# Optimization experiments

Hardware: AMD Instinct MI355X
Metric: run time of the kernel (lower is better)

The kernel has to match this reference:

```python
import jax, jax.numpy as jnp
import numpy as np

B, S, D, H = 64, 256, 2048, 8
DH = D // H  # 256; NOTE: S must equal DH for the original module's broadcast to be valid
EPS = 1e-06


def setup_inputs() -> dict:
    key = jax.random.key(0)
    ks = jax.random.split(key, 8)
    s = 1.0 / np.sqrt(D)
    x = jax.random.normal(ks[0], (B, S, D), jnp.float32)
    Wq = jax.random.normal(ks[1], (D, D), jnp.float32) * s
    Wk = jax.random.normal(ks[2], (D, D), jnp.float32) * s
    Wv = jax.random.normal(ks[3], (D, D), jnp.float32) * s
    Wo = jax.random.normal(ks[4], (2 * D, D), jnp.float32) * (1.0 / np.sqrt(2 * D))
    bq = jnp.zeros((D,), jnp.float32)
    bk = jnp.zeros((D,), jnp.float32)
    bv = jnp.zeros((D,), jnp.float32)
    bo = jnp.zeros((D,), jnp.float32)
    gamma = jnp.ones((D,), jnp.float32)
    beta = jnp.zeros((D,), jnp.float32)
    return {"x": x, "Wq": Wq, "bq": bq, "Wk": Wk, "bk": bk, "Wv": Wv, "bv": bv,
            "Wo": Wo, "bo": bo, "gamma": gamma, "beta": beta}


def reference(x, Wq, bq, Wk, bk, Wv, bv, Wo, bo, gamma, beta):
    def split_heads(t):  # [B,S,D] -> [B,H,S,DH]
        return t.reshape(B, S, H, DH).transpose(0, 2, 1, 3)

    q_proj = x @ Wq + bq  # reused later as the residual projection
    q = jax.nn.elu(split_heads(q_proj)) + 1.0
    k = jax.nn.elu(split_heads(x @ Wk + bk)) + 1.0
    v = split_heads(x @ Wv + bv)

    key_sum = k.sum(axis=2, keepdims=True)  # [B,H,1,DH]
    # Original TF code broadcasts [B,H,S,S] / [B,H,1,DH]; valid because S == DH
    scores = jnp.einsum('bhqd,bhkd->bhqk', q, k) / (key_sum + EPS)
    attn = jnp.einsum('bhqk,bhkd->bhqd', scores, v)
    attn = attn.transpose(0, 2, 1, 3).reshape(B, S, D)

    summary = jnp.broadcast_to(attn.mean(axis=1, keepdims=True), (B, S, D))
    combined = jnp.concatenate([attn, summary], axis=-1) @ Wo + bo  # [B,S,D]
    # dropout is identity (training=False)

    z = q_proj + combined
    mu = z.mean(axis=-1, keepdims=True)
    var = z.var(axis=-1, keepdims=True)
    return (z - mu) / jnp.sqrt(var + EPS) * gamma + beta
```

## Files before the change

kernel.cpp:

```cpp
#include <hip/hip_runtime.h>
#include <hip/hip_bf16.h>

typedef __attribute__((ext_vector_type(8))) __bf16 bf16x8v;
typedef __attribute__((ext_vector_type(4))) float f32x4;
typedef __attribute__((ext_vector_type(4))) unsigned short u16x4;
typedef __attribute__((ext_vector_type(8))) unsigned short u16x8;

#define LN_EPS 1e-6f

__device__ __forceinline__ unsigned short f2bf(float f) {
  union { float f; unsigned int u; } v; v.f = f;
  unsigned int r = v.u + 0x7fffu + ((v.u >> 16) & 1u);
  return (unsigned short)(r >> 16);
}
__device__ __forceinline__ float bf2f(unsigned short u) {
  union { unsigned int u; float f; } v; v.u = ((unsigned int)u) << 16;
  return v.f;
}
__device__ __forceinline__ float elu1(float x) {
  return x > 0.f ? x + 1.f : __expf(x);
}
__device__ __forceinline__ void gload16(const void* g, void* l) {
  __builtin_amdgcn_global_load_lds((__attribute__((address_space(1))) void*)g,
                                   (__attribute__((address_space(3))) void*)l,
                                   16, 0, 0);
}

__global__ __launch_bounds__(256) void cvt_f32_bf16(const float* __restrict__ in,
                                                    unsigned short* __restrict__ out, long n) {
  long stride = (long)gridDim.x * 256 * 8;
  for (long i = ((long)blockIdx.x * 256 + threadIdx.x) * 8; i < n; i += stride) {
    float4 a = *(const float4*)(in + i);
    float4 b = *(const float4*)(in + i + 4);
    u16x8 o;
    o[0] = f2bf(a.x); o[1] = f2bf(a.y); o[2] = f2bf(a.z); o[3] = f2bf(a.w);
    o[4] = f2bf(b.x); o[5] = f2bf(b.y); o[6] = f2bf(b.z); o[7] = f2bf(b.w);
    *(u16x8*)(out + i) = o;
  }
}

struct Tr4Args { const float* src[4]; unsigned short* dst[4]; };
__global__ __launch_bounds__(256) void tr_cvt4(Tr4Args t4) {
  __shared__ float t[64][65];
  const float* in = t4.src[blockIdx.z];
  unsigned short* out = t4.dst[blockIdx.z];
  int r0 = blockIdx.y * 64, c0 = blockIdx.x * 64;
  for (int idx = threadIdx.x; idx < 4096; idx += 256) {
    int r = idx >> 6, c = idx & 63;
    t[r][c] = in[(long)(r0 + r) * 2048 + c0 + c];
  }
  __syncthreads();
  for (int idx = threadIdx.x; idx < 4096; idx += 256) {
    int c = idx >> 6, r = idx & 63;
    out[(long)(c0 + c) * 2048 + r0 + r] = f2bf(t[r][c]);
  }
}

__global__ __launch_bounds__(256) void colsum_bf16(const unsigned short* __restrict__ in,
                                                   float* __restrict__ out, int rows, float scale) {
  int b = blockIdx.y;
  int col = blockIdx.x * 256 + threadIdx.x;
  const unsigned short* p = in + (long)b * rows * 2048 + col;
  float acc = 0.f;
  for (int s = 0; s < rows; ++s) acc += bf2f(p[(long)s * 2048]);
  out[(long)b * 2048 + col] = acc * scale;
}

__global__ __launch_bounds__(256) void srow_part(const float* __restrict__ summ,
                                                 const float* __restrict__ Wo2,
                                                 float* __restrict__ part) {
  int col = blockIdx.x * 256 + threadIdx.x;
  int b = blockIdx.y;
  int k0 = blockIdx.z * 256;
  const float* s = summ + (long)b * 2048 + k0;
  const float* w = Wo2 + (long)k0 * 2048 + col;
  float acc = 0.f;
#pragma unroll 8
  for (int k = 0; k < 256; ++k) acc += s[k] * w[(long)k * 2048];
  part[((long)blockIdx.z * 64 + b) * 2048 + col] = acc;
}
__global__ __launch_bounds__(256) void srow_sum(const float* __restrict__ part,
                                                float* __restrict__ srow) {
  int col = blockIdx.x * 256 + threadIdx.x;
  int b = blockIdx.y;
  float acc = 0.f;
#pragma unroll
  for (int kb = 0; kb < 8; ++kb) acc += part[((long)kb * 64 + b) * 2048 + col];
  srow[(long)b * 2048 + col] = acc;
}

__global__ __launch_bounds__(256) void ln_k(const unsigned short* __restrict__ z,
                                            const float* __restrict__ gamma,
                                            const float* __restrict__ beta,
                                            float* __restrict__ out) {
  long row = blockIdx.x;
  int t = threadIdx.x;
  u16x8 zv = *(const u16x8*)(z + row * 2048 + t * 8);
  float zf[8];
  float s = 0.f, q = 0.f;
#pragma unroll
  for (int j = 0; j < 8; ++j) {
    zf[j] = bf2f(zv[j]);
    s += zf[j];
    q += zf[j] * zf[j];
  }
#pragma unroll
  for (int o = 32; o >= 1; o >>= 1) { s += __shfl_xor(s, o); q += __shfl_xor(q, o); }
  __shared__ float ss[4], qq[4];
  if ((t & 63) == 0) { ss[t >> 6] = s; qq[t >> 6] = q; }
  __syncthreads();
  s = ss[0] + ss[1] + ss[2] + ss[3];
  q = qq[0] + qq[1] + qq[2] + qq[3];
  float mu = s * (1.f / 2048.f);
  float var = q * (1.f / 2048.f) - mu * mu;
  float rstd = rsqrtf(var + LN_EPS);
  float4 g1 = *(const float4*)(gamma + t * 8);
  float4 g2 = *(const float4*)(gamma + t * 8 + 4);
  float4 b1 = *(const float4*)(beta + t * 8);
  float4 b2 = *(const float4*)(beta + t * 8 + 4);
  float4 o1, o2;
  o1.x = (zf[0] - mu) * rstd * g1.x + b1.x;
  o1.y = (zf[1] - mu) * rstd * g1.y + b1.y;
  o1.z = (zf[2] - mu) * rstd * g1.z + b1.z;
  o1.w = (zf[3] - mu) * rstd * g1.w + b1.w;
  o2.x = (zf[4] - mu) * rstd * g2.x + b2.x;
  o2.y = (zf[5] - mu) * rstd * g2.y + b2.y;
  o2.z = (zf[6] - mu) * rstd * g2.z + b2.z;
  o2.w = (zf[7] - mu) * rstd * g2.w + b2.w;
  *(float4*)(out + row * 2048 + t * 8) = o1;
  *(float4*)(out + row * 2048 + t * 8 + 4) = o2;
}

struct GemmArgs {
  const unsigned short* A; long lda, sAb, sAh;
  const unsigned short* B; long ldb, sBb, sBh;
  char* C; long ldc, sCb, sCh;
  int K;
  const float* aux; long sXb, sXh;
  const unsigned short* residb;
  const float* srow;
  unsigned short* out2;
  const float* bk2;
  const float* bv2;
  unsigned short* kact2;
  unsigned short* vt2;
};

template <int EPI>
__device__ __forceinline__ void epi_frag(const GemmArgs& g, char* Cb, int bz, int hz,
                                         long grow0, long gcol, f32x4 v) {
  if (EPI == 6) {
    const int wsel = (int)(gcol >> 11);
    const long cw = gcol & 2047;
    if (wsel == 0) {
      const float bias = g.aux[cw];
      unsigned short* Ch = (unsigned short*)Cb;
#pragma unroll
      for (int rr = 0; rr < 4; ++rr) {
        const long idx = (grow0 + rr) * 2048 + cw;
        const float vv = v[rr] + bias;
        Ch[idx] = f2bf(vv);
        g.out2[idx] = f2bf(elu1(vv));
      }
    } else if (wsel == 1) {
      const float bias = g.bk2[cw];
#pragma unroll
      for (int rr = 0; rr < 4; ++rr)
        g.kact2[(grow0 + rr) * 2048 + cw] = f2bf(elu1(v[rr] + bias));
    } else {
      const float bias = g.bv2[cw];
      const long batch = grow0 >> 8;
      const int sloc = (int)(grow0 & 255);
      u16x4 pk;
#pragma unroll
      for (int rr = 0; rr < 4; ++rr) pk[rr] = f2bf(v[rr] + bias);
      *(u16x4*)(g.vt2 + (batch * 2048 + cw) * 256 + sloc) = pk;
    }
  } else if (EPI == 3) {
    const float* divs = g.aux + bz * g.sXb + hz * g.sXh;
    const float d = divs[gcol] + LN_EPS;
    unsigned short* Ch = (unsigned short*)Cb;
#pragma unroll
    for (int rr = 0; rr < 4; ++rr)
      Ch[(grow0 + rr) * g.ldc + gcol] = f2bf(v[rr] / d);
  } else if (EPI == 4) {
    unsigned short* Ch = (unsigned short*)Cb;
#pragma unroll
    for (int rr = 0; rr < 4; ++rr)
      Ch[(grow0 + rr) * g.ldc + gcol] = f2bf(v[rr]);
  } else {
    const float bias = g.aux[gcol];
    unsigned short* Ch = (unsigned short*)Cb;
#pragma unroll
    for (int rr = 0; rr < 4; ++rr) {
      const long grow = grow0 + rr;
      const long idx = grow * g.ldc + gcol;
      const float vv = v[rr] + bias + bf2f(g.residb[idx]) + g.srow[(grow >> 8) * 2048 + gcol];
      Ch[idx] = f2bf(vv);
    }
  }
}

template <int EPI>
__global__ __launch_bounds__(256, 4) void gemm_bt(GemmArgs g) {
  const int tid = threadIdx.x;
  const int lane = tid & 63;
  const int wave = tid >> 6;
  const int wm = wave >> 1, wn = wave & 1;
  const int bz = (int)blockIdx.z >> 3, hz = (int)blockIdx.z & 7;
  const long mBase = (long)blockIdx.x * 128;
  const long nBase = (long)blockIdx.y * 128;
  const unsigned short* Ab = g.A + bz * g.sAb + hz * g.sAh;
  const unsigned short* Bb = g.B + bz * g.sBb + hz * g.sBh;

  __shared__ __align__(16) unsigned short Asm[128 * 64];
  __shared__ __align__(16) unsigned short Bsm[128 * 64];

  f32x4 acc[4][4] = {};

  for (int kt = 0; kt < g.K; kt += 64) {
#pragma unroll
    for (int i = 0; i < 4; ++i) {
      const int u = i * 256 + tid;
      const int rr = u >> 3;
      const int cc = (((u & 7) ^ (rr & 7)) << 3);
      gload16(Ab + (mBase + rr) * g.lda + kt + cc, Asm + (size_t)u * 8);
      gload16(Bb + (nBase + rr) * g.ldb + kt + cc, Bsm + (size_t)u * 8);
    }
    __syncthreads();
#pragma unroll
    for (int ks = 0; ks < 64; ks += 32) {
      const int kof = ks + ((lane >> 4) << 3);
      bf16x8v a[4], b[4];
#pragma unroll
      for (int mi = 0; mi < 4; ++mi) {
        const int row = wm * 64 + mi * 16 + (lane & 15);
        a[mi] = *(const bf16x8v*)&Asm[row * 64 + (kof ^ ((row & 7) << 3))];
      }
#pragma unroll
      for (int ni = 0; ni < 4; ++ni) {
        const int row = wn * 64 + ni * 16 + (lane & 15);
        b[ni] = *(const bf16x8v*)&Bsm[row * 64 + (kof ^ ((row & 7) << 3))];
      }
#pragma unroll
      for (int mi = 0; mi < 4; ++mi)
#pragma unroll
        for (int ni = 0; ni < 4; ++ni)
          acc[mi][ni] = __builtin_amdgcn_mfma_f32_16x16x32_bf16(a[mi], b[ni], acc[mi][ni], 0, 0, 0);
    }
    __syncthreads();
  }

  char* Cb = g.C + bz * g.sCb + hz * g.sCh;
#pragma unroll
  for (int mi = 0; mi < 4; ++mi) {
    const long grow0 = mBase + wm * 64 + mi * 16 + ((lane >> 4) << 2);
#pragma unroll
    for (int ni = 0; ni < 4; ++ni)
      epi_frag<EPI>(g, Cb, bz, hz, grow0, nBase + wn * 64 + ni * 16 + (lane & 15), acc[mi][ni]);
  }
}

extern "C" void kernel_launch(void* const* d_in, const int* in_sizes, int n_in,
                              void* d_out, int out_size, void* d_ws, size_t ws_size,
                              hipStream_t stream) {
  (void)in_sizes; (void)n_in; (void)out_size;
  const float* x     = (const float*)d_in[0];
  const float* Wq    = (const float*)d_in[1];
  const float* bq    = (const float*)d_in[2];
  const float* Wk    = (const float*)d_in[3];
  const float* bk    = (const float*)d_in[4];
  const float* Wv    = (const float*)d_in[5];
  const float* bv    = (const float*)d_in[6];
  const float* Wo    = (const float*)d_in[7];
  const float* bo    = (const float*)d_in[8];
  const float* gamma = (const float*)d_in[9];
  const float* beta  = (const float*)d_in[10];
  float* out = (float*)d_out;

  const long M = 16384, D = 2048;
  char* ws = (char*)d_ws;
  size_t o = 0;
  unsigned short* xbf = (unsigned short*)(ws + o); o += (size_t)M * D * 2;
  unsigned short* wqT = (unsigned short*)(ws + o); o += (size_t)D * D * 2;
  unsigned short* wkT = (unsigned short*)(ws + o); o += (size_t)D * D * 2;
  unsigned short* wvT = (unsigned short*)(ws + o); o += (size_t)D * D * 2;
  unsigned short* woT = (unsigned short*)(ws + o); o += (size_t)D * D * 2;
  unsigned short* qpro = (unsigned short*)(ws + o); o += (size_t)M * D * 2;
  unsigned short* qact = (unsigned short*)(ws + o); o += (size_t)M * D * 2;
  unsigned short* kact = (unsigned short*)(ws + o); o += (size_t)M * D * 2;
  unsigned short* vT   = (unsigned short*)(ws + o); o += (size_t)M * D * 2;
  unsigned short* P    = (unsigned short*)(ws + o); o += (size_t)512 * 65536 * 2;
  float* ksum = (float*)(ws + o); o += (size_t)64 * 2048 * 4;
  float* summ = (float*)(ws + o); o += (size_t)64 * 2048 * 4;
  float* srow = (float*)(ws + o); o += (size_t)64 * 2048 * 4;
  unsigned short* attn = xbf;
  float* spart = (float*)P;
  if (ws_size < o) return;

  cvt_f32_bf16<<<2048, 256, 0, stream>>>(x, xbf, M * D);
  Tr4Args t4;
  t4.src[0] = Wq; t4.src[1] = Wk; t4.src[2] = Wv; t4.src[3] = Wo;
  t4.dst[0] = wqT; t4.dst[1] = wkT; t4.dst[2] = wvT; t4.dst[3] = woT;
  tr_cvt4<<<dim3(32, 32, 4), 256, 0, stream>>>(t4);

  GemmArgs a{};
  a.A = xbf; a.lda = 2048; a.sAb = 0; a.sAh = 0;
  a.B = wqT; a.ldb = 2048; a.sBb = 0; a.sBh = 0;
  a.C = (char*)qpro; a.ldc = 2048; a.sCb = 0; a.sCh = 0;
  a.K = 2048; a.aux = bq; a.sXb = 0; a.sXh = 0;
  a.residb = nullptr; a.srow = nullptr; a.out2 = qact;
  a.bk2 = bk; a.bv2 = bv; a.kact2 = kact; a.vt2 = vT;
  gemm_bt<6><<<dim3(128, 48, 1), 256, 0, stream>>>(a);

  colsum_bf16<<<dim3(8, 64), 256, 0, stream>>>(kact, ksum, 256, 1.0f);

  GemmArgs sA{};
  sA.A = qact; sA.lda = 2048; sA.sAb = 256 * 2048; sA.sAh = 256;
  sA.B = kact; sA.ldb = 2048; sA.sBb = 256 * 2048; sA.sBh = 256;
  sA.C = (char*)P; sA.ldc = 256; sA.sCb = 8L * 65536 * 2; sA.sCh = 65536L * 2;
  sA.K = 256; sA.aux = ksum; sA.sXb = 2048; sA.sXh = 256;
  sA.residb = nullptr; sA.srow = nullptr; sA.out2 = nullptr;
  gemm_bt<3><<<dim3(2, 2, 512), 256, 0, stream>>>(sA);

  GemmArgs tA{};
  tA.A = P; tA.lda = 256; tA.sAb = 8L * 65536; tA.sAh = 65536;
  tA.B = vT; tA.ldb = 256; tA.sBb = 2048L * 256; tA.sBh = 256 * 256;
  tA.C = (char*)attn; tA.ldc = 2048; tA.sCb = 256L * 2048 * 2; tA.sCh = 256 * 2;
  tA.K = 256; tA.aux = nullptr; tA.sXb = 0; tA.sXh = 0;
  tA.residb = nullptr; tA.srow = nullptr; tA.out2 = nullptr;
  gemm_bt<4><<<dim3(2, 2, 512), 256, 0, stream>>>(tA);

  colsum_bf16<<<dim3(8, 64), 256, 0, stream>>>(attn, summ, 256, 1.0f / 256.0f);
  srow_part<<<dim3(8, 64, 8), 256, 0, stream>>>(summ, Wo + (size_t)2048 * 2048, spart);
  srow_sum<<<dim3(8, 64), 256, 0, stream>>>(spart, srow);

  GemmArgs zA{};
  zA.A = attn; zA.lda = 2048; zA.sAb = 0; zA.sAh = 0;
  zA.B = woT; zA.ldb = 2048; zA.sBb = 0; zA.sBh = 0;
  zA.C = (char*)qpro; zA.ldc = 2048; zA.sCb = 0; zA.sCh = 0;
  zA.K = 2048; zA.aux = bo; zA.sXb = 0; zA.sXh = 0;
  zA.residb = qpro; zA.srow = srow; zA.out2 = nullptr;
  gemm_bt<5><<<dim3(128, 16, 1), 256, 0, stream>>>(zA);

  ln_k<<<16384, 256, 0, stream>>>(qpro, gamma, beta, out);
}
```

Measured before the change: 1.035 ms.

## Use 256x256 eight-wave pipelined GEMM for fused QKV projection

Result: slower. 1.059 ms (+2.3%).

```diff
diff --git a/kernel.cpp b/kernel.cpp
--- a/kernel.cpp
+++ b/kernel.cpp
@@ -261,6 +261,136 @@
   }
 }
 
+template <int EPI>
+__global__ __launch_bounds__(512, 2) void gemm8p(GemmArgs g) {
+  const int tid = threadIdx.x;
+  const int lane = tid & 63;
+  const int wave = tid >> 6;
+  const int wm = wave >> 2;
+  const int wn = wave & 3;
+  const long mBase = (long)blockIdx.x * 256;
+  const long nBase = (long)blockIdx.y * 256;
+  const unsigned short* Ab = g.A + mBase * g.lda;
+  const unsigned short* Bb = g.B + nBase * g.ldb;
+
+  __shared__ __align__(16) unsigned short Asm[2][2][128 * 64];
+  __shared__ __align__(16) unsigned short Bsm[2][2][128 * 64];
+
+  f32x4 acc[8][4] = {};
+  bf16x8v a[4][2], b[2][2];
+  const int nt = g.K >> 6;
+  const int lrow = lane & 15;
+  const int kof0 = (lane >> 4) << 3;
+  const int lxor = (lane & 7) << 3;
+
+#define STAGE_A(buf, mh, kt)                                                     \
+  {                                                                              \
+    _Pragma("unroll")                                                            \
+    for (int j = 0; j < 2; ++j) {                                                \
+      const int u = j * 512 + tid;                                               \
+      const int rl = u >> 3;                                                     \
+      const long r = rl + (rl & 64) + (mh) * 64;                                 \
+      const int cc = (((u & 7) ^ (rl & 7)) << 3);                                \
+      gload16(Ab + r * g.lda + (kt) + cc, &Asm[buf][mh][(size_t)u * 8]);         \
+    }                                                                            \
+  }
+#define STAGE_B(buf, nh, kt)                                                     \
+  {                                                                              \
+    _Pragma("unroll")                                                            \
+    for (int j = 0; j < 2; ++j) {                                                \
+      const int u = j * 512 + tid;                                               \
+      const int rl = u >> 3;                                                     \
+      const long r = rl + (rl & 96) + (nh) * 32;                                 \
+      const int cc = (((u & 7) ^ (rl & 7)) << 3);                                \
+      gload16(Bb + r * g.ldb + (kt) + cc, &Bsm[buf][nh][(size_t)u * 8]);         \
+    }                                                                            \
+  }
+#define LOAD_A(buf, mh)                                                          \
+  {                                                                              \
+    _Pragma("unroll")                                                            \
+    for (int mi = 0; mi < 4; ++mi) {                                             \
+      const int rl = wm * 64 + mi * 16 + lrow;                                   \
+      _Pragma("unroll")                                                          \
+      for (int ks = 0; ks < 2; ++ks)                                             \
+        a[mi][ks] = *(const bf16x8v*)&Asm[buf][mh][rl * 64 + ((ks * 32 + kof0) ^ lxor)]; \
+    }                                                                            \
+  }
+#define LOAD_B(buf, nh)                                                          \
+  {                                                                              \
+    _Pragma("unroll")                                                            \
+    for (int ni = 0; ni < 2; ++ni) {                                             \
+      const int rl = wn * 32 + ni * 16 + lrow;                                   \
+      _Pragma("unroll")                                                          \
+      for (int ks = 0; ks < 2; ++ks)                                             \
+        b[ni][ks] = *(const bf16x8v*)&Bsm[buf][nh][rl * 64 + ((ks * 32 + kof0) ^ lxor)]; \
+    }                                                                            \
+  }
+#define MFMA_Q(mh, nh)                                                           \
+  {                                                                              \
+    __builtin_amdgcn_s_setprio(1);                                               \
+    _Pragma("unroll")                                                            \
+    for (int mi = 0; mi < 4; ++mi)                                               \
+      _Pragma("unroll")                                                          \
+      for (int ni = 0; ni < 2; ++ni)                                             \
+        _Pragma("unroll")                                                        \
+        for (int ks = 0; ks < 2; ++ks)                                           \
+          acc[(mh) * 4 + mi][(nh) * 2 + ni] = __builtin_amdgcn_mfma_f32_16x16x32_bf16( \
+              a[mi][ks], b[ni][ks], acc[(mh) * 4 + mi][(nh) * 2 + ni], 0, 0, 0); \
+    __builtin_amdgcn_s_setprio(0);                                               \
+  }
+#define BAR()  __builtin_amdgcn_s_barrier(); asm volatile("" ::: "memory");
+#define LGKM() asm volatile("s_waitcnt lgkmcnt(0)" ::: "memory"); \
+               __builtin_amdgcn_sched_barrier(0);
+
+  STAGE_A(0, 0, 0); STAGE_B(0, 1, 0); STAGE_A(0, 1, 0); STAGE_B(0, 0, 0);
+  asm volatile("s_waitcnt vmcnt(0)" ::: "memory");
+  BAR();
+  STAGE_A(1, 0, 64); STAGE_B(1, 1, 64); STAGE_A(1, 1, 64);
+
+  for (int t = 0; t < nt; ++t) {
+    const int cb = t & 1, nb = cb ^ 1;
+    const int kt2 = (t + 2) << 6;
+    LOAD_A(cb, 0); LOAD_B(cb, 0);
+    if (t + 1 < nt) STAGE_B(nb, 0, (t + 1) << 6);
+    BAR(); LGKM();
+    MFMA_Q(0, 0);
+    BAR();
+    LOAD_B(cb, 1);
+    if (t + 2 < nt) STAGE_A(cb, 0, kt2);
+    BAR(); LGKM();
+    MFMA_Q(0, 1);
+    BAR();
+    LOAD_A(cb, 1);
+    if (t + 2 < nt) STAGE_B(cb, 1, kt2);
+    BAR(); LGKM();
+    MFMA_Q(1, 1);
+    BAR();
+    LOAD_B(cb, 0);
+    if (t + 2 < nt) STAGE_A(cb, 1, kt2);
+    BAR(); LGKM();
+    MFMA_Q(1, 0);
+    if (t < nt - 2)       { asm volatile("s_waitcnt vmcnt(6)" ::: "memory"); }
+    else if (t == nt - 2) { asm volatile("s_waitcnt vmcnt(0)" ::: "memory"); }
+    BAR();
+  }
+#undef STAGE_A
+#undef STAGE_B
+#undef LOAD_A
+#undef LOAD_B
+#undef MFMA_Q
+#undef BAR
+#undef LGKM
+
+  char* Cb = g.C;
+#pragma unroll
+  for (int fi = 0; fi < 8; ++fi) {
+    const long grow0 = mBase + wm * 128 + fi * 16 + ((lane >> 4) << 2);
+#pragma unroll
+    for (int fj = 0; fj < 4; ++fj)
+      epi_frag<EPI>(g, Cb, 0, 0, grow0, nBase + wn * 64 + fj * 16 + (lane & 15), acc[fi][fj]);
+  }
+}
+
 extern "C" void kernel_launch(void* const* d_in, const int* in_sizes, int n_in,
                               void* d_out, int out_size, void* d_ws, size_t ws_size,
                               hipStream_t stream) {
@@ -311,7 +441,7 @@
   a.K = 2048; a.aux = bq; a.sXb = 0; a.sXh = 0;
   a.residb = nullptr; a.srow = nullptr; a.out2 = qact;
   a.bk2 = bk; a.bv2 = bv; a.kact2 = kact; a.vt2 = vT;
-  gemm_bt<6><<<dim3(128, 48, 1), 256, 0, stream>>>(a);
+  gemm8p<6><<<dim3(64, 24), 512, 0, stream>>>(a);
 
   colsum_bf16<<<dim3(8, 64), 256, 0, stream>>>(kact, ksum, 256, 1.0f);
 
```
